# Performance work log

Measured on AMD Instinct MI355X. Metric: run time of the kernel, lower is better.

## Reference

```python
import jax, jax.numpy as jnp
import numpy as np

B, N, E, H, T, FC = 16, 4096, 131072, 16, 3, 20


def setup_inputs() -> dict:
    key = jax.random.key(0)
    ks = jax.random.split(key, 16)
    F = jnp.eye(3, dtype=jnp.float32)[None] + 0.05 * jax.random.normal(ks[0], (B, 3, 3), dtype=jnp.float32)
    node_pos = jax.random.uniform(ks[1], (N, 3), dtype=jnp.float32)
    edge_src = jax.random.randint(ks[2], (E,), 0, N)
    edge_dst = jax.random.randint(ks[3], (E,), 0, N)
    edge_type = jax.random.randint(ks[4], (E,), 0, T)
    sc = lambda k, s: jax.random.normal(k, s, dtype=jnp.float32) / np.float32(np.sqrt(s[0]))
    return {
        'F': F, 'node_pos': node_pos,
        'edge_src': edge_src, 'edge_dst': edge_dst, 'edge_type': edge_type,
        'W_in': sc(ks[5], (3, H)),
        'fc1_0': sc(ks[6], (T, FC)), 'fc2_0': sc(ks[7], (FC, 1)), 'W_0': sc(ks[8], (H, H)),
        'fc1_1': sc(ks[9], (T, FC)), 'fc2_1': sc(ks[10], (FC, 1)), 'W_1': sc(ks[11], (H, H)),
        'W_out': sc(ks[12], (H, 3)),
        'w': jax.random.uniform(ks[13], (N * N,), dtype=jnp.float32),
    }


def _message_passing(Fx, edge_src, edge_dst, edge_oh,
                     W_in, fc1_0, fc2_0, W_0, fc1_1, fc2_1, W_1, W_out):
    # simplified stand-in for e3nn MessagePassing_v1: per-edge scalar gate from
    # edge-type MLP (fc_neurons=[3,20]), gather-scatter aggregation / sqrt(deg)
    inv_sqrt_deg = np.float32(1.0 / np.sqrt(edge_src.shape[0] / Fx.shape[1]))
    h = Fx @ W_in  # [B,N,H]
    for fc1, fc2, Wl in ((fc1_0, fc2_0, W_0), (fc1_1, fc2_1, W_1)):
        ew = jax.nn.relu(edge_oh @ fc1) @ fc2          # [E,1]
        msg = h[:, edge_src] * ew[None]                # [B,E,H]
        agg = jnp.zeros_like(h).at[:, edge_dst].add(msg) * inv_sqrt_deg
        h = jax.nn.relu(agg @ Wl)
    return h @ W_out  # [B,N,3]


def reference(F, node_pos, edge_src, edge_dst, edge_type,
              W_in, fc1_0, fc2_0, W_0, fc1_1, fc2_1, W_1, W_out, w):
    edge_oh = jax.nn.one_hot(edge_type, T, dtype=F.dtype)
    Fx = jnp.einsum('bij,nj->bni', F, node_pos)                     # deform positions
    h = _message_passing(Fx, edge_src, edge_dst, edge_oh,
                         W_in, fc1_0, fc2_0, W_0, fc1_1, fc2_1, W_1, W_out)
    Fx_ij = h[:, edge_src] - h[:, edge_dst]                         # [B,E,3]
    x_ij = jnp.einsum('bij,bej->bei', jnp.linalg.inv(F), Fx_ij)     # [B,E,3]
    n = node_pos.shape[0]
    a = Fx_ij[:, :n]  # original loop indexes first N edges with node index i
    c = x_ij[:, :n]
    W2 = w.reshape(n, n)
    # vectorized form of: sum_ij w[i*n+j] * kron(Fx_ij[b,i], x_ij[b,j])
    t = jnp.einsum('ij,bip->bjp', W2, a)                            # [B,N,3]
    stress = jnp.einsum('bjp,bjq->bpq', t, c).reshape(F.shape[0], 9)
    return stress
```

## Files before the change

kernel.cpp:

```cpp
#include <hip/hip_runtime.h>

#define N_NODES 4096
#define N_EDGES 131072
#define BATCH   16
#define HDIM    16
#define FCDIM   20
#define BH      256
#define ISD     0.17677669529663687f
#define NSTRIP  32

__device__ __forceinline__ float f4get(const float4& v, int k) {
    return k == 0 ? v.x : (k == 1 ? v.y : (k == 2 ? v.z : v.w));
}

__global__ void setup_kernel(const float* __restrict__ F, const float* __restrict__ W_in,
                             const float* __restrict__ fc1_0, const float* __restrict__ fc2_0,
                             const float* __restrict__ fc1_1, const float* __restrict__ fc2_1,
                             float* __restrict__ ew, float* __restrict__ G,
                             float* __restrict__ invF, float* __restrict__ out144,
                             int* __restrict__ cnt) {
    int t = threadIdx.x;
    if (t < 6) {
        const float* fc1 = (t < 3) ? fc1_0 : fc1_1;
        const float* fc2 = (t < 3) ? fc2_0 : fc2_1;
        int ty = t % 3;
        float s = 0.f;
        for (int f = 0; f < FCDIM; ++f) {
            float v = fc1[ty * FCDIM + f];
            v = v > 0.f ? v : 0.f;
            s += v * fc2[f];
        }
        ew[t] = s;
    }
    for (int idx = t; idx < BATCH * 3 * HDIM; idx += 256) {
        int b = idx / 48, r = idx % 48, j = r / HDIM, k = r % HDIM;
        float s = 0.f;
        for (int i = 0; i < 3; ++i) s += F[b * 9 + i * 3 + j] * W_in[i * HDIM + k];
        G[idx] = s;
    }
    if (t < BATCH) {
        const float* f = F + t * 9;
        float a00=f[0],a01=f[1],a02=f[2],a10=f[3],a11=f[4],a12=f[5],a20=f[6],a21=f[7],a22=f[8];
        float det = a00*(a11*a22-a12*a21) - a01*(a10*a22-a12*a20) + a02*(a10*a21-a11*a20);
        float id = 1.f/det;
        float* o = invF + t*9;
        o[0]=(a11*a22-a12*a21)*id; o[1]=(a02*a21-a01*a22)*id; o[2]=(a01*a12-a02*a11)*id;
        o[3]=(a12*a20-a10*a22)*id; o[4]=(a00*a22-a02*a20)*id; o[5]=(a02*a10-a00*a12)*id;
        o[6]=(a10*a21-a11*a20)*id; o[7]=(a01*a20-a00*a21)*id; o[8]=(a00*a11-a01*a10)*id;
    }
    if (t < 144) out144[t] = 0.f;
    for (int i = t; i < N_NODES; i += 256) cnt[i] = 0;
}

__global__ void h0_hist_kernel(const float* __restrict__ pos, const float* __restrict__ G,
                               float* __restrict__ h0,
                               const int* __restrict__ edst, int* __restrict__ cnt) {
    int bid = blockIdx.x;
    int t = threadIdx.x;
    if (bid < 1024) {
        int id = bid * 256 + t;
        int n  = id >> 6;
        int c4 = (id & 63) << 2;
        int b  = c4 >> 4;
        int k  = c4 & 15;
        float p0 = pos[n*3+0], p1 = pos[n*3+1], p2 = pos[n*3+2];
        const float* g = G + b*48 + k;
        float4 r;
        r.x = p0*g[0] + p1*g[16] + p2*g[32];
        r.y = p0*g[1] + p1*g[17] + p2*g[33];
        r.z = p0*g[2] + p1*g[18] + p2*g[34];
        r.w = p0*g[3] + p1*g[19] + p2*g[35];
        *(float4*)(h0 + n*BH + c4) = r;
    } else {
        int e = (bid - 1024) * 256 + t;
        if (e < N_EDGES) atomicAdd(&cnt[edst[e]], 1);
    }
}

__global__ void scan_kernel(const int* __restrict__ cnt, int* __restrict__ off,
                            int* __restrict__ cursor) {
    __shared__ int wsum[4];
    int t = threadIdx.x;
    int lane = t & 63, wave = t >> 6;
    int base = t * 16;
    int loc[16];
    int s = 0;
    #pragma unroll
    for (int i = 0; i < 16; ++i) { loc[i] = s; s += cnt[base + i]; }
    int pre = s;
    #pragma unroll
    for (int o = 1; o < 64; o <<= 1) {
        int v = __shfl_up(pre, o);
        if (lane >= o) pre += v;
    }
    if (lane == 63) wsum[wave] = pre;
    __syncthreads();
    int woff = 0;
    #pragma unroll
    for (int w = 0; w < 4; ++w) if (w < wave) woff += wsum[w];
    int excl = woff + pre - s;
    #pragma unroll
    for (int i = 0; i < 16; ++i) {
        int v = excl + loc[i];
        off[base + i] = v;
        cursor[base + i] = v;
    }
    if (t == 255) off[N_NODES] = excl + s;
}
__global__ void fill_kernel(const int* __restrict__ src, const int* __restrict__ dst,
                            const int* __restrict__ typ, int* __restrict__ cursor,
                            int* __restrict__ sedge) {
    int e = blockIdx.x * 256 + threadIdx.x;
    if (e < N_EDGES) {
        int p = atomicAdd(&cursor[dst[e]], 1);
        sedge[p] = src[e] | (typ[e] << 16);
    }
}

__global__ void layer_kernel(const float* __restrict__ h_in, float* __restrict__ h_out,
                             const int* __restrict__ off, const int* __restrict__ sedge,
                             const float* __restrict__ ew3, const float* __restrict__ W) {
    __shared__ float Wl[256];
    __shared__ float aggS[2][16*17 + 4];
    int t = threadIdx.x;
    Wl[t] = W[t];
    int wave = t >> 6, lane = t & 63;
    int node = wave >> 1;
    int half = wave & 1;
    int d = blockIdx.x * 2 + node;
    float e0 = ew3[0], e1 = ew3[1], e2 = ew3[2];
    int beg = off[d], end = off[d+1];
    int col = half * 128 + lane * 2;
    float2 acc = {0.f, 0.f};
    int it = beg;
    for (; it + 7 < end; it += 8) {
        int v[8]; float2 hv[8];
        #pragma unroll
        for (int u = 0; u < 8; ++u) v[u] = sedge[it + u];
        #pragma unroll
        for (int u = 0; u < 8; ++u)
            hv[u] = *(const float2*)(h_in + (v[u] & 0xFFFF) * BH + col);
        #pragma unroll
        for (int u = 0; u < 8; ++u) {
            int ty = v[u] >> 16;
            float wg = (ty == 0) ? e0 : (ty == 1 ? e1 : e2);
            acc.x += wg * hv[u].x; acc.y += wg * hv[u].y;
        }
    }
    for (; it < end; ++it) {
        int v = sedge[it];
        int ty = v >> 16;
        float wg = (ty == 0) ? e0 : (ty == 1 ? e1 : e2);
        float2 hv = *(const float2*)(h_in + (v & 0xFFFF) * BH + col);
        acc.x += wg * hv.x; acc.y += wg * hv.y;
    }
    int b = col >> 4, k0 = col & 15;
    aggS[node][b*17 + k0]     = acc.x * ISD;
    aggS[node][b*17 + k0 + 1] = acc.y * ISD;
    __syncthreads();
    int en = t >> 7, c2 = (t & 127) * 2;
    int eb = c2 >> 4, ek = c2 & 15;
    const float* arow = aggS[en] + eb * 17;
    float o0 = 0.f, o1 = 0.f;
    #pragma unroll
    for (int k = 0; k < 16; ++k) {
        float av = arow[k];
        o0 += av * Wl[k*16 + ek];
        o1 += av * Wl[k*16 + ek + 1];
    }
    int ed = blockIdx.x * 2 + en;
    float2 r;
    r.x = o0 > 0.f ? o0 : 0.f;
    r.y = o1 > 0.f ? o1 : 0.f;
    *(float2*)(h_out + ed*BH + c2) = r;
}

__global__ void hout_kernel(const float* __restrict__ h2, const float* __restrict__ Wout,
                            float* __restrict__ hout) {
    __shared__ float Wo[48];
    int t = threadIdx.x;
    if (t < 48) Wo[t] = Wout[t];
    __syncthreads();
    int id = blockIdx.x * 256 + t;
    int n = id >> 4, b = id & 15;
    const float* hr = h2 + n*BH + b*HDIM;
    float s0=0.f, s1=0.f, s2=0.f;
    #pragma unroll
    for (int k = 0; k < 16; ++k) {
        float v = hr[k];
        s0 += v*Wo[k*3+0]; s1 += v*Wo[k*3+1]; s2 += v*Wo[k*3+2];
    }
    float* o = hout + n*48 + b*3;
    o[0]=s0; o[1]=s1; o[2]=s2;
}

__global__ void ac_kernel(const float* __restrict__ hout, const int* __restrict__ esrc,
                          const int* __restrict__ edst, const float* __restrict__ invF,
                          float* __restrict__ a, float* __restrict__ c) {
    __shared__ float iF[144];
    int t = threadIdx.x;
    if (t < 144) iF[t] = invF[t];
    __syncthreads();
    int id = blockIdx.x * 256 + t;
    int i = id >> 4, b = id & 15;
    int s = esrc[i], d = edst[i];
    float a0 = hout[s*48+b*3+0] - hout[d*48+b*3+0];
    float a1 = hout[s*48+b*3+1] - hout[d*48+b*3+1];
    float a2 = hout[s*48+b*3+2] - hout[d*48+b*3+2];
    float* ap = a + i*48 + b*3;
    ap[0]=a0; ap[1]=a1; ap[2]=a2;
    const float* m = iF + b*9;
    float* cp = c + i*48 + b*3;
    cp[0] = m[0]*a0 + m[1]*a1 + m[2]*a2;
    cp[1] = m[3]*a0 + m[4]*a1 + m[5]*a2;
    cp[2] = m[6]*a0 + m[7]*a1 + m[8]*a2;
}

__global__ __launch_bounds__(256, 4)
void tmat_kernel(const float* __restrict__ W2, const float* __restrict__ a,
                 float* __restrict__ partial) {
    __shared__ float sa[128 * 48];
    int t = threadIdx.x;
    int lane = t & 63;
    int wave = t >> 6;
    int cg   = wave * 12;
    int jb    = (blockIdx.x & 31) * 128;
    int strip = blockIdx.x >> 5;
    int i0    = strip * 128;
    {
        const float4* ga = (const float4*)(a + (size_t)i0 * 48);
        float4* la = (float4*)sa;
        #pragma unroll
        for (int k = 0; k < 6; ++k) la[t + k * 256] = ga[t + k * 256];
    }
    __syncthreads();
    int j = jb + lane * 2;
    const float* w2p = W2 + (size_t)i0 * N_NODES + j;
    float4 acc[2][3];
    #pragma unroll
    for (int jj = 0; jj < 2; ++jj)
        #pragma unroll
        for (int q = 0; q < 3; ++q) acc[jj][q] = make_float4(0.f,0.f,0.f,0.f);
    float2 w[8];
    #pragma unroll
    for (int u = 0; u < 8; ++u)
        w[u] = *(const float2*)(w2p + (size_t)u * N_NODES);
    #pragma unroll 1
    for (int base = 0; base < 128; base += 8) {
        float2 wn[8];
        #pragma unroll
        for (int u = 0; u < 8; ++u) {
            int r = base + 8 + u; if (r > 127) r = 127;
            wn[u] = *(const float2*)(w2p + (size_t)r * N_NODES);
        }
        #pragma unroll
        for (int u = 0; u < 8; ++u) {
            const float* ar = &sa[(base + u) * 48 + cg];
            float4 x = *(const float4*)(ar);
            float4 y = *(const float4*)(ar + 4);
            float4 z = *(const float4*)(ar + 8);
            #pragma unroll
            for (int jj = 0; jj < 2; ++jj) {
                float wv = jj == 0 ? w[u].x : w[u].y;
                acc[jj][0].x += wv*x.x; acc[jj][0].y += wv*x.y;
                acc[jj][0].z += wv*x.z; acc[jj][0].w += wv*x.w;
                acc[jj][1].x += wv*y.x; acc[jj][1].y += wv*y.y;
                acc[jj][1].z += wv*y.z; acc[jj][1].w += wv*y.w;
                acc[jj][2].x += wv*z.x; acc[jj][2].y += wv*z.y;
                acc[jj][2].z += wv*z.z; acc[jj][2].w += wv*z.w;
            }
        }
        #pragma unroll
        for (int u = 0; u < 8; ++u) w[u] = wn[u];
    }
    float* pbase = partial + (size_t)strip * (48 * N_NODES) + jb;
    #pragma unroll
    for (int c = 0; c < 12; ++c) {
        float2 v;
        v.x = f4get(acc[0][c >> 2], c & 3);
        v.y = f4get(acc[1][c >> 2], c & 3);
        *(float2*)(pbase + (size_t)(cg + c) * N_NODES + lane * 2) = v;
    }
}

__global__ void reduce_kernel(const float* __restrict__ partial, float* __restrict__ tmat) {
    int x = (blockIdx.x * 64 + threadIdx.x) * 4;
    float4 s = {0.f, 0.f, 0.f, 0.f};
    #pragma unroll 4
    for (int st = 0; st < NSTRIP; ++st) {
        float4 v = *(const float4*)(partial + (size_t)st * (48 * N_NODES) + x);
        s.x += v.x; s.y += v.y; s.z += v.z; s.w += v.w;
    }
    *(float4*)(tmat + x) = s;
}

__global__ void stress2_kernel(const float* __restrict__ tmat, const float* __restrict__ c,
                               float* __restrict__ out) {
    __shared__ float shred[256 * 9];
    int t = threadIdx.x;
    int b = t & 15, jl = t >> 4;
    int jbase = blockIdx.x * 64;
    float s[9];
    #pragma unroll
    for (int r = 0; r < 9; ++r) s[r] = 0.f;
    for (int pass = 0; pass < 4; ++pass) {
        int j = jbase + pass * 16 + jl;
        float t0 = tmat[(size_t)(b*3+0) * N_NODES + j];
        float t1 = tmat[(size_t)(b*3+1) * N_NODES + j];
        float t2 = tmat[(size_t)(b*3+2) * N_NODES + j];
        const float* cp = c + (size_t)j * 48 + b * 3;
        float c0 = cp[0], c1 = cp[1], c2 = cp[2];
        s[0] += t0*c0; s[1] += t0*c1; s[2] += t0*c2;
        s[3] += t1*c0; s[4] += t1*c1; s[5] += t1*c2;
        s[6] += t2*c0; s[7] += t2*c1; s[8] += t2*c2;
    }
    #pragma unroll
    for (int r = 0; r < 9; ++r) shred[t * 9 + r] = s[r];
    __syncthreads();
    if (t < 144) {
        int bb = t / 9, r = t % 9;
        float acc = 0.f;
        #pragma unroll
        for (int g = 0; g < 16; ++g)
            acc += shred[(g * 16 + bb) * 9 + r];
        atomicAdd(&out[t], acc);
    }
}

extern "C" void kernel_launch(void* const* d_in, const int* in_sizes, int n_in,
                              void* d_out, int out_size, void* d_ws, size_t ws_size,
                              hipStream_t stream) {
    const float* F     = (const float*)d_in[0];
    const float* pos   = (const float*)d_in[1];
    const int*   esrc  = (const int*)d_in[2];
    const int*   edst  = (const int*)d_in[3];
    const int*   etyp  = (const int*)d_in[4];
    const float* W_in  = (const float*)d_in[5];
    const float* fc1_0 = (const float*)d_in[6];
    const float* fc2_0 = (const float*)d_in[7];
    const float* W_0   = (const float*)d_in[8];
    const float* fc1_1 = (const float*)d_in[9];
    const float* fc2_1 = (const float*)d_in[10];
    const float* W_1   = (const float*)d_in[11];
    const float* W_out = (const float*)d_in[12];
    const float* w2    = (const float*)d_in[13];
    float* out = (float*)d_out;

    float* ws   = (float*)d_ws;
    float* ew   = ws;
    float* G    = ws + 16;
    float* invF = ws + 800;
    float* bufA = ws + 1024;
    float* bufB = bufA + N_NODES*BH;
    float* hout = bufB + N_NODES*BH;
    float* aArr = hout + N_NODES*48;
    float* cArr = aArr + N_NODES*48;
    float* tmat = cArr + N_NODES*48;
    int* cnt    = (int*)(tmat + N_NODES*48);
    int* off    = cnt + N_NODES;
    int* cursor = off + N_NODES + 1;
    int* sedge  = cursor + N_NODES;
    float* partial = (float*)(sedge + N_EDGES);

    setup_kernel<<<1, 256, 0, stream>>>(F, W_in, fc1_0, fc2_0, fc1_1, fc2_1, ew, G, invF, out, cnt);
    h0_hist_kernel<<<1536, 256, 0, stream>>>(pos, G, bufA, edst, cnt);
    scan_kernel<<<1, 256, 0, stream>>>(cnt, off, cursor);
    fill_kernel<<<512, 256, 0, stream>>>(esrc, edst, etyp, cursor, sedge);
    layer_kernel<<<2048, 256, 0, stream>>>(bufA, bufB, off, sedge, ew,     W_0);
    layer_kernel<<<2048, 256, 0, stream>>>(bufB, bufA, off, sedge, ew + 3, W_1);
    hout_kernel<<<256, 256, 0, stream>>>(bufA, W_out, hout);
    ac_kernel<<<256, 256, 0, stream>>>(hout, esrc, edst, invF, aArr, cArr);
    tmat_kernel<<<1024, 256, 0, stream>>>(w2, aArr, partial);
    reduce_kernel<<<768, 64, 0, stream>>>(partial, tmat);
    stress2_kernel<<<64, 256, 0, stream>>>(tmat, cArr, out);
}
```

Measured before the change: 215.9 us.

## Fuse tmat, strip reduction and stress contraction into one kernel

The per-strip partial products of W2 with the a array are no longer written to a 32-way partial buffer and then reduced and contracted in two more kernels. Each block now loads its c tile into padded shared memory, contracts its accumulators against c directly, reduces across the wavefront with shuffles, and atomically adds into the 144 output values. The W2 prefetch is also deepened to 16 rows per iteration. This removes about 25 MB of partial-buffer traffic and two launches, at the cost of more registers, an occupancy hint lowered from 4 to 3, many shuffle reductions and 36 atomics per wave onto only 144 addresses.

```diff
diff --git a/kernel.cpp b/kernel.cpp
--- a/kernel.cpp
+++ b/kernel.cpp
@@ -7,7 +7,6 @@
 #define FCDIM   20
 #define BH      256
 #define ISD     0.17677669529663687f
-#define NSTRIP  32
 
 __device__ __forceinline__ float f4get(const float4& v, int k) {
     return k == 0 ? v.x : (k == 1 ? v.y : (k == 2 ? v.z : v.w));
@@ -216,10 +215,11 @@
     cp[2] = m[6]*a0 + m[7]*a1 + m[8]*a2;
 }
 
-__global__ __launch_bounds__(256, 4)
-void tmat_kernel(const float* __restrict__ W2, const float* __restrict__ a,
-                 float* __restrict__ partial) {
+__global__ __launch_bounds__(256, 3)
+void stress_fused_kernel(const float* __restrict__ W2, const float* __restrict__ a,
+                         const float* __restrict__ c, float* __restrict__ out) {
     __shared__ float sa[128 * 48];
+    __shared__ float sc[128 * 49];
     int t = threadIdx.x;
     int lane = t & 63;
     int wave = t >> 6;
@@ -233,6 +233,17 @@
         #pragma unroll
         for (int k = 0; k < 6; ++k) la[t + k * 256] = ga[t + k * 256];
     }
+    {
+        const float4* gc = (const float4*)(c + (size_t)jb * 48);
+        #pragma unroll
+        for (int k = 0; k < 6; ++k) {
+            int id4 = t + k * 256;
+            float4 v = gc[id4];
+            int jl = (id4 * 4) / 48, col = (id4 * 4) % 48;
+            float* d = &sc[jl * 49 + col];
+            d[0] = v.x; d[1] = v.y; d[2] = v.z; d[3] = v.w;
+        }
+    }
     __syncthreads();
     int j = jb + lane * 2;
     const float* w2p = W2 + (size_t)i0 * N_NODES + j;
@@ -241,17 +252,25 @@
     for (int jj = 0; jj < 2; ++jj)
         #pragma unroll
         for (int q = 0; q < 3; ++q) acc[jj][q] = make_float4(0.f,0.f,0.f,0.f);
-    float2 w[8];
+    float2 wa[8], wb[8];
     #pragma unroll
     for (int u = 0; u < 8; ++u)
-        w[u] = *(const float2*)(w2p + (size_t)u * N_NODES);
+        wa[u] = *(const float2*)(w2p + (size_t)u * N_NODES);
+    #pragma unroll
+    for (int u = 0; u < 8; ++u)
+        wb[u] = *(const float2*)(w2p + (size_t)(8 + u) * N_NODES);
     #pragma unroll 1
-    for (int base = 0; base < 128; base += 8) {
-        float2 wn[8];
-        #pragma unroll
-        for (int u = 0; u < 8; ++u) {
-            int r = base + 8 + u; if (r > 127) r = 127;
-            wn[u] = *(const float2*)(w2p + (size_t)r * N_NODES);
+    for (int base = 0; base < 128; base += 16) {
+        float2 wa2[8], wb2[8];
+        #pragma unroll
+        for (int u = 0; u < 8; ++u) {
+            int r = base + 16 + u; if (r > 127) r = 127;
+            wa2[u] = *(const float2*)(w2p + (size_t)r * N_NODES);
+        }
+        #pragma unroll
+        for (int u = 0; u < 8; ++u) {
+            int r = base + 24 + u; if (r > 127) r = 127;
+            wb2[u] = *(const float2*)(w2p + (size_t)r * N_NODES);
         }
         #pragma unroll
         for (int u = 0; u < 8; ++u) {
@@ -261,7 +280,7 @@
             float4 z = *(const float4*)(ar + 8);
             #pragma unroll
             for (int jj = 0; jj < 2; ++jj) {
-                float wv = jj == 0 ? w[u].x : w[u].y;
+                float wv = jj == 0 ? wa[u].x : wa[u].y;
                 acc[jj][0].x += wv*x.x; acc[jj][0].y += wv*x.y;
                 acc[jj][0].z += wv*x.z; acc[jj][0].w += wv*x.w;
                 acc[jj][1].x += wv*y.x; acc[jj][1].y += wv*y.y;
@@ -271,59 +290,57 @@
             }
         }
         #pragma unroll
-        for (int u = 0; u < 8; ++u) w[u] = wn[u];
-    }
-    float* pbase = partial + (size_t)strip * (48 * N_NODES) + jb;
-    #pragma unroll
-    for (int c = 0; c < 12; ++c) {
-        float2 v;
-        v.x = f4get(acc[0][c >> 2], c & 3);
-        v.y = f4get(acc[1][c >> 2], c & 3);
-        *(float2*)(pbase + (size_t)(cg + c) * N_NODES + lane * 2) = v;
-    }
-}
-
-__global__ void reduce_kernel(const float* __restrict__ partial, float* __restrict__ tmat) {
-    int x = (blockIdx.x * 64 + threadIdx.x) * 4;
-    float4 s = {0.f, 0.f, 0.f, 0.f};
-    #pragma unroll 4
-    for (int st = 0; st < NSTRIP; ++st) {
-        float4 v = *(const float4*)(partial + (size_t)st * (48 * N_NODES) + x);
-        s.x += v.x; s.y += v.y; s.z += v.z; s.w += v.w;
-    }
-    *(float4*)(tmat + x) = s;
-}
-
-__global__ void stress2_kernel(const float* __restrict__ tmat, const float* __restrict__ c,
-                               float* __restrict__ out) {
-    __shared__ float shred[256 * 9];
-    int t = threadIdx.x;
-    int b = t & 15, jl = t >> 4;
-    int jbase = blockIdx.x * 64;
-    float s[9];
-    #pragma unroll
-    for (int r = 0; r < 9; ++r) s[r] = 0.f;
-    for (int pass = 0; pass < 4; ++pass) {
-        int j = jbase + pass * 16 + jl;
-        float t0 = tmat[(size_t)(b*3+0) * N_NODES + j];
-        float t1 = tmat[(size_t)(b*3+1) * N_NODES + j];
-        float t2 = tmat[(size_t)(b*3+2) * N_NODES + j];
-        const float* cp = c + (size_t)j * 48 + b * 3;
-        float c0 = cp[0], c1 = cp[1], c2 = cp[2];
-        s[0] += t0*c0; s[1] += t0*c1; s[2] += t0*c2;
-        s[3] += t1*c0; s[4] += t1*c1; s[5] += t1*c2;
-        s[6] += t2*c0; s[7] += t2*c1; s[8] += t2*c2;
-    }
-    #pragma unroll
-    for (int r = 0; r < 9; ++r) shred[t * 9 + r] = s[r];
-    __syncthreads();
-    if (t < 144) {
-        int bb = t / 9, r = t % 9;
-        float acc = 0.f;
-        #pragma unroll
-        for (int g = 0; g < 16; ++g)
-            acc += shred[(g * 16 + bb) * 9 + r];
-        atomicAdd(&out[t], acc);
+        for (int u = 0; u < 8; ++u) {
+            const float* ar = &sa[(base + 8 + u) * 48 + cg];
+            float4 x = *(const float4*)(ar);
+            float4 y = *(const float4*)(ar + 4);
+            float4 z = *(const float4*)(ar + 8);
+            #pragma unroll
+            for (int jj = 0; jj < 2; ++jj) {
+                float wv = jj == 0 ? wb[u].x : wb[u].y;
+                acc[jj][0].x += wv*x.x; acc[jj][0].y += wv*x.y;
+                acc[jj][0].z += wv*x.z; acc[jj][0].w += wv*x.w;
+                acc[jj][1].x += wv*y.x; acc[jj][1].y += wv*y.y;
+                acc[jj][1].z += wv*y.z; acc[jj][1].w += wv*y.w;
+                acc[jj][2].x += wv*z.x; acc[jj][2].y += wv*z.y;
+                acc[jj][2].z += wv*z.z; acc[jj][2].w += wv*z.w;
+            }
+        }
+        #pragma unroll
+        for (int u = 0; u < 8; ++u) { wa[u] = wa2[u]; wb[u] = wb2[u]; }
+    }
+    float s[36];
+    #pragma unroll
+    for (int m = 0; m < 36; ++m) s[m] = 0.f;
+    #pragma unroll
+    for (int jj = 0; jj < 2; ++jj) {
+        const float* cvp = &sc[(lane * 2 + jj) * 49 + cg];
+        float cv[12];
+        #pragma unroll
+        for (int m = 0; m < 12; ++m) cv[m] = cvp[m];
+        #pragma unroll
+        for (int cc = 0; cc < 12; ++cc) {
+            float tv = f4get(acc[jj][cc >> 2], cc & 3);
+            int qb = (cc / 3) * 3;
+            s[cc*3+0] += tv * cv[qb+0];
+            s[cc*3+1] += tv * cv[qb+1];
+            s[cc*3+2] += tv * cv[qb+2];
+        }
+    }
+    #pragma unroll
+    for (int m = 0; m < 36; ++m) {
+        float v = s[m];
+        #pragma unroll
+        for (int o = 1; o < 64; o <<= 1) v += __shfl_xor(v, o);
+        s[m] = v;
+    }
+    if (lane == 0) {
+        #pragma unroll
+        for (int m = 0; m < 36; ++m) {
+            int cc = m / 3, q = m % 3;
+            int bp = cg + cc;
+            atomicAdd(&out[(bp / 3) * 9 + (bp % 3) * 3 + q], s[m]);
+        }
     }
 }
 
@@ -355,12 +372,10 @@
     float* hout = bufB + N_NODES*BH;
     float* aArr = hout + N_NODES*48;
     float* cArr = aArr + N_NODES*48;
-    float* tmat = cArr + N_NODES*48;
-    int* cnt    = (int*)(tmat + N_NODES*48);
+    int* cnt    = (int*)(cArr + N_NODES*48);
     int* off    = cnt + N_NODES;
     int* cursor = off + N_NODES + 1;
     int* sedge  = cursor + N_NODES;
-    float* partial = (float*)(sedge + N_EDGES);
 
     setup_kernel<<<1, 256, 0, stream>>>(F, W_in, fc1_0, fc2_0, fc1_1, fc2_1, ew, G, invF, out, cnt);
     h0_hist_kernel<<<1536, 256, 0, stream>>>(pos, G, bufA, edst, cnt);
@@ -370,7 +385,5 @@
     layer_kernel<<<2048, 256, 0, stream>>>(bufB, bufA, off, sedge, ew + 3, W_1);
     hout_kernel<<<256, 256, 0, stream>>>(bufA, W_out, hout);
     ac_kernel<<<256, 256, 0, stream>>>(hout, esrc, edst, invF, aArr, cArr);
-    tmat_kernel<<<1024, 256, 0, stream>>>(w2, aArr, partial);
-    reduce_kernel<<<768, 64, 0, stream>>>(partial, tmat);
-    stress2_kernel<<<64, 256, 0, stream>>>(tmat, cArr, out);
-}
+    stress_fused_kernel<<<1024, 256, 0, stream>>>(w2, aArr, cArr, out);
+}
```

Result: slower. 591.9 us (+174.2%).
